# Performance work log

Hardware: AMD Instinct MI355X
Metric: run time of the kernel (lower is better)

Reference implementation:

```python
import jax, jax.numpy as jnp
import numpy as np

B = 4096      # number of snakes (graphs)
L = 256       # fixed snake length (nodes per chain)
N = B * L     # total nodes
HID = 32
OUT = 32
AUX = 32
FIN = 64
N_FRUITS = 1
AUX_IN = 2 + 1 + N_FRUITS * 2  # = 5


def _chain_edges():
    # chain edges i<->i+1 within each graph, both directions (PyG undirected chain)
    base = np.arange(L - 1)
    src1 = (np.arange(B)[:, None] * L + base[None, :]).ravel()
    dst1 = src1 + 1
    src = np.concatenate([src1, dst1])
    dst = np.concatenate([dst1, src1])
    return np.stack([src, dst]).astype(np.int64)  # [2, 2*(L-1)*B]


def setup_inputs() -> dict:
    key = jax.random.key(0)
    ks = jax.random.split(key, 16)

    def lin(k, fan_in, fan_out):
        k1, k2 = jax.random.split(k)
        bound = 1.0 / np.sqrt(fan_in)
        W = jax.random.uniform(k1, (fan_in, fan_out), jnp.float32, -bound, bound)
        b = jax.random.uniform(k2, (fan_out,), jnp.float32, -bound, bound)
        return W, b

    x = jax.random.normal(ks[0], (N, 2), jnp.float32)
    heads = jax.random.normal(ks[1], (B, 2), jnp.float32)
    body_sizes = jax.random.uniform(ks[2], (B, 1), jnp.float32)
    fruits = jax.random.normal(ks[3], (B, N_FRUITS, 2), jnp.float32)

    W1, b1 = lin(ks[4], 2, HID)
    W2, b2 = lin(ks[5], HID, HID)
    Wr, br = lin(ks[6], HID, OUT)
    Wa1, ba1 = lin(ks[7], AUX_IN, AUX)
    Wa2, ba2 = lin(ks[8], AUX, AUX)
    Wc, bc = lin(ks[9], OUT + AUX, FIN)
    Wp, bp = lin(ks[10], FIN, 5)
    Wv, bv = lin(ks[11], FIN, 1)

    edge_index = jnp.asarray(_chain_edges())
    batch_ids = jnp.repeat(jnp.arange(B, dtype=jnp.int64), L)

    return dict(x=x, heads=heads, body_sizes=body_sizes, fruits=fruits,
                W1=W1, b1=b1, W2=W2, b2=b2, Wr=Wr, br=br,
                Wa1=Wa1, ba1=ba1, Wa2=Wa2, ba2=ba2, Wc=Wc, bc=bc,
                Wp=Wp, bp=bp, Wv=Wv, bv=bv,
                edge_index=edge_index, batch_ids=batch_ids)


def _gcn_conv(h, W, b, src, dst):
    # PyG GCNConv: out = D^{-1/2} (A + I) D^{-1/2} (h W) + b, deg counts self-loop
    h = h @ W  # [N, F]
    ones = jnp.ones(src.shape[0], h.dtype)
    deg = jax.ops.segment_sum(ones, dst, num_segments=N) + 1.0  # self-loop
    dinv = jax.lax.rsqrt(deg)
    norm = dinv[src] * dinv[dst]  # [E]
    agg = jax.ops.segment_sum(norm[:, None] * h[src], dst, num_segments=N)
    agg = agg + (dinv * dinv)[:, None] * h  # self-loop messages
    return agg + b


def reference(x, heads, body_sizes, fruits,
              W1, b1, W2, b2, Wr, br, Wa1, ba1, Wa2, ba2,
              Wc, bc, Wp, bp, Wv, bv, edge_index, batch_ids):
    src, dst = edge_index[0], edge_index[1]
    h = jax.nn.relu(_gcn_conv(x, W1, b1, src, dst))
    h = jax.nn.relu(_gcn_conv(h, W2, b2, src, dst))
    # global mean pool per graph
    pooled = jax.ops.segment_sum(h, batch_ids, num_segments=B)
    counts = jax.ops.segment_sum(jnp.ones(N, h.dtype), batch_ids, num_segments=B)
    pooled = pooled / counts[:, None]
    body_emb = pooled @ Wr + br  # [B, OUT]

    aux_input = jnp.concatenate([heads, body_sizes,
                                 fruits.reshape(fruits.shape[0], -1)], axis=-1)
    aux = jax.nn.relu(aux_input @ Wa1 + ba1)
    aux = jax.nn.relu(aux @ Wa2 + ba2)

    combined = jnp.concatenate([body_emb, aux], axis=-1)
    combined = jax.nn.relu(combined @ Wc + bc)
    logits = combined @ Wp + bp  # [B, 5]
    value = combined @ Wv + bv   # [B, 1]
    return logits, value
```

## Files before the change

kernel.cpp:

```cpp
#include <hip/hip_runtime.h>
#include <hip/hip_bf16.h>


#define NB  4096
#define CL  256
#define HID 32
#define FIN 64
#define SPB 4

typedef __attribute__((ext_vector_type(8))) short    bf16x8;
typedef __attribute__((ext_vector_type(4))) float    f32x4;
typedef __attribute__((ext_vector_type(4))) unsigned u32x4;

__device__ __forceinline__ unsigned pkbf(float a, float b) {
    __hip_bfloat162 hb = __float22bfloat162_rn(make_float2(a, b));
    unsigned u; __builtin_memcpy(&u, &hb, sizeof(u));
    return u;
}
__device__ __forceinline__ float bflo(unsigned u) { return __builtin_bit_cast(float, u << 16); }
__device__ __forceinline__ float bfhi(unsigned u) { return __builtin_bit_cast(float, u & 0xffff0000u); }

__device__ __forceinline__ void gcn_coef(int n, float& nc, float& nl, float& nr) {
    const float IS3 = 0.57735026918962576f, IS2 = 0.70710678118654752f;
    const float dn = (n == 0 || n == CL - 1) ? IS2 : IS3;
    nc = dn * dn;
    nl = (n > 0)      ? dn * ((n == 1)      ? IS2 : IS3) : 0.0f;
    nr = (n < CL - 1) ? dn * ((n == CL - 2) ? IS2 : IS3) : 0.0f;
}

__global__ __launch_bounds__(256, 4) void snake_fused(
    const float* __restrict__ x,
    const float* __restrict__ heads,
    const float* __restrict__ body_sizes,
    const float* __restrict__ fruits,
    const float* __restrict__ W1, const float* __restrict__ b1,
    const float* __restrict__ W2, const float* __restrict__ b2,
    const float* __restrict__ Wr, const float* __restrict__ br,
    const float* __restrict__ Wa1, const float* __restrict__ ba1,
    const float* __restrict__ Wa2, const float* __restrict__ ba2,
    const float* __restrict__ Wc, const float* __restrict__ bc,
    const float* __restrict__ Wp, const float* __restrict__ bp,
    const float* __restrict__ Wv, const float* __restrict__ bv,
    float* __restrict__ out)
{
    __shared__ __align__(16) float edgebuf[SPB][4][2][HID];
    __shared__ __align__(16) float waveparts[SPB][HID][4];
    __shared__ __align__(16) float poolLDS[SPB][HID];
    __shared__ __align__(16) float auxLDS[SPB][HID];
    __shared__ __align__(16) float catLDS[SPB][FIN];

    const int blk  = blockIdx.x;
    const int i    = threadIdx.x;
    const int w    = i >> 6;
    const int lane = i & 63;
    const int g    = lane >> 4;
    const int c    = lane & 15;

    bf16x8 Bh[2], Bl[2];
    #pragma unroll
    for (int nt = 0; nt < 2; ++nt) {
        unsigned hh[4], ll[4];
        #pragma unroll
        for (int p = 0; p < 4; ++p) {
            const float wa = W2[(8 * g + 2 * p)     * HID + c + 16 * nt];
            const float wb = W2[(8 * g + 2 * p + 1) * HID + c + 16 * nt];
            const unsigned hu = pkbf(wa, wb);
            hh[p] = hu;
            ll[p] = pkbf(wa - bflo(hu), wb - bfhi(hu));
        }
        u32x4 H = {hh[0], hh[1], hh[2], hh[3]};
        u32x4 L = {ll[0], ll[1], ll[2], ll[3]};
        Bh[nt] = __builtin_bit_cast(bf16x8, H);
        Bl[nt] = __builtin_bit_cast(bf16x8, L);
    }
    const float b2v0 = b2[c], b2v1 = b2[c + 16];

    const float4 W1a0 = *reinterpret_cast<const float4*>(W1 + 8 * g);
    const float4 W1a1 = *reinterpret_cast<const float4*>(W1 + 8 * g + 4);
    const float4 W1b0 = *reinterpret_cast<const float4*>(W1 + HID + 8 * g);
    const float4 W1b1 = *reinterpret_cast<const float4*>(W1 + HID + 8 * g + 4);
    const float4 b1v0 = *reinterpret_cast<const float4*>(b1 + 8 * g);
    const float4 b1v1 = *reinterpret_cast<const float4*>(b1 + 8 * g + 4);

    float ncd, nld, nrd;
    gcn_coef(i, ncd, nld, nrd);

    const float THIRD = 0.33333333333333333f;
    const float I23   = 0.40824829046386302f;
    const bool fixL = (w == 0) && (g == 0);
    const bool fixR = (w == 3) && (g == 3);

    #pragma unroll 1
    for (int s = 0; s < SPB; ++s) {
        const int gs = SPB * blk + s;
        const float2* xs = reinterpret_cast<const float2*>(x) + gs * CL;

        const float2 xc = xs[i];
        const float2 xl = xs[i - (i > 0)];
        const float2 xr = xs[i + (i < CL - 1)];
        const float sxx = ncd * xc.x + nld * xl.x + nrd * xr.x;
        const float sxy = ncd * xc.y + nld * xl.y + nrd * xr.y;

        float sxA[4], syA[4];
        #pragma unroll
        for (int t = 0; t < 4; ++t) {
            sxA[t] = __shfl(sxx, 16 * t + c, 64);
            syA[t] = __shfl(sxy, 16 * t + c, 64);
        }

        f32x4 acc[4][2];
        #pragma unroll
        for (int t = 0; t < 4; ++t)
            #pragma unroll
            for (int nt = 0; nt < 2; ++nt) { f32x4 z = {0.f, 0.f, 0.f, 0.f}; acc[t][nt] = z; }

        #pragma unroll
        for (int t = 0; t < 4; ++t) {
            const float sa = sxA[t], sb = syA[t];
            const float r0 = fmaxf(fmaf(sa, W1a0.x, fmaf(sb, W1b0.x, b1v0.x)), 0.f);
            const float r1 = fmaxf(fmaf(sa, W1a0.y, fmaf(sb, W1b0.y, b1v0.y)), 0.f);
            const float r2 = fmaxf(fmaf(sa, W1a0.z, fmaf(sb, W1b0.z, b1v0.z)), 0.f);
            const float r3 = fmaxf(fmaf(sa, W1a0.w, fmaf(sb, W1b0.w, b1v0.w)), 0.f);
            const float r4 = fmaxf(fmaf(sa, W1a1.x, fmaf(sb, W1b1.x, b1v1.x)), 0.f);
            const float r5 = fmaxf(fmaf(sa, W1a1.y, fmaf(sb, W1b1.y, b1v1.y)), 0.f);
            const float r6 = fmaxf(fmaf(sa, W1a1.z, fmaf(sb, W1b1.z, b1v1.z)), 0.f);
            const float r7 = fmaxf(fmaf(sa, W1a1.w, fmaf(sb, W1b1.w, b1v1.w)), 0.f);
            const unsigned h0 = pkbf(r0, r1), h1 = pkbf(r2, r3);
            const unsigned h2 = pkbf(r4, r5), h3 = pkbf(r6, r7);
            const unsigned q0 = pkbf(r0 - bflo(h0), r1 - bfhi(h0));
            const unsigned q1 = pkbf(r2 - bflo(h1), r3 - bfhi(h1));
            const unsigned q2 = pkbf(r4 - bflo(h2), r5 - bfhi(h2));
            const unsigned q3 = pkbf(r6 - bflo(h3), r7 - bfhi(h3));
            u32x4 HU = {h0, h1, h2, h3};
            u32x4 LU = {q0, q1, q2, q3};
            const bf16x8 ah = __builtin_bit_cast(bf16x8, HU);
            const bf16x8 al = __builtin_bit_cast(bf16x8, LU);
            #pragma unroll
            for (int nt = 0; nt < 2; ++nt) {
                acc[t][nt] = __builtin_amdgcn_mfma_f32_16x16x32_bf16(ah, Bh[nt], acc[t][nt], 0, 0, 0);
                acc[t][nt] = __builtin_amdgcn_mfma_f32_16x16x32_bf16(al, Bh[nt], acc[t][nt], 0, 0, 0);
                acc[t][nt] = __builtin_amdgcn_mfma_f32_16x16x32_bf16(ah, Bl[nt], acc[t][nt], 0, 0, 0);
            }
        }

        if (lane < 16) {
            edgebuf[s][w][0][c]      = acc[0][0][0];
            edgebuf[s][w][0][c + 16] = acc[0][1][0];
        } else if (lane >= 48) {
            edgebuf[s][w][1][c]      = acc[3][0][3];
            edgebuf[s][w][1][c + 16] = acc[3][1][3];
        }
        __syncthreads();

        float sum0 = 0.f, sum1 = 0.f;
        #pragma unroll
        for (int t = 0; t < 4; ++t) {
            float c0 = THIRD, r0c = THIRD, l1c = THIRD;
            float c3 = THIRD, l3c = THIRD, r2c = THIRD;
            if (t == 0) { c0 = fixL ? 0.5f : THIRD; r0c = fixL ? I23 : THIRD; l1c = fixL ? I23 : THIRD; }
            if (t == 3) { c3 = fixR ? 0.5f : THIRD; l3c = fixR ? I23 : THIRD; r2c = fixR ? I23 : THIRD; }
            #pragma unroll
            for (int nt = 0; nt < 2; ++nt) {
                const f32x4 v = acc[t][nt];
                const float Lsend = (g == 3) ? acc[(t > 0) ? t - 1 : 0][nt][3] : acc[t][nt][3];
                const int   Lsrc  = (g == 0) ? (c + 48) : (lane - 16);
                float L = __shfl(Lsend, Lsrc, 64);
                if (t == 0) {
                    float eL = edgebuf[s][(w > 0) ? w - 1 : 0][1][c + 16 * nt];
                    eL = (w > 0) ? eL : 0.f;
                    L = (g == 0) ? eL : L;
                }
                const float Rsend = (g == 0) ? acc[(t < 3) ? t + 1 : 3][nt][0] : acc[t][nt][0];
                const int   Rsrc  = (g == 3) ? c : (lane + 16);
                float R = __shfl(Rsend, Rsrc, 64);
                if (t == 3) {
                    float eR = edgebuf[s][(w < 3) ? w + 1 : 3][0][c + 16 * nt];
                    eR = (w < 3) ? eR : 0.f;
                    R = (g == 3) ? eR : R;
                }
                const float bb = (nt == 0) ? b2v0 : b2v1;
                const float h0 = fmaxf(fmaf(c0,    v[0], fmaf(THIRD, L,    fmaf(r0c,  v[1], bb))), 0.f);
                const float h1 = fmaxf(fmaf(THIRD, v[1], fmaf(l1c,   v[0], fmaf(THIRD, v[2], bb))), 0.f);
                const float h2 = fmaxf(fmaf(THIRD, v[2], fmaf(THIRD, v[1], fmaf(r2c,  v[3], bb))), 0.f);
                const float h3 = fmaxf(fmaf(c3,    v[3], fmaf(l3c,   v[2], fmaf(THIRD, R,   bb))), 0.f);
                const float hs = (h0 + h1) + (h2 + h3);
                if (nt == 0) sum0 += hs; else sum1 += hs;
            }
        }
        sum0 += __shfl_xor(sum0, 16, 64); sum0 += __shfl_xor(sum0, 32, 64);
        sum1 += __shfl_xor(sum1, 16, 64); sum1 += __shfl_xor(sum1, 32, 64);
        if (g == 0) {
            waveparts[s][c][w]      = sum0;
            waveparts[s][c + 16][w] = sum1;
        }
    }
    __syncthreads();

    const int gsH = SPB * blk + w;
    if (lane < HID) {
        const f32x4 wp = *reinterpret_cast<const f32x4*>(&waveparts[w][lane][0]);
        poolLDS[w][lane] = (wp.x + wp.y + wp.z + wp.w) * (1.0f / CL);
    } else {
        const int cc = lane - HID;
        float a = ba1[cc];
        a = fmaf(heads[2 * gsH],      Wa1[0 * HID + cc], a);
        a = fmaf(heads[2 * gsH + 1],  Wa1[1 * HID + cc], a);
        a = fmaf(body_sizes[gsH],     Wa1[2 * HID + cc], a);
        a = fmaf(fruits[2 * gsH],     Wa1[3 * HID + cc], a);
        a = fmaf(fruits[2 * gsH + 1], Wa1[4 * HID + cc], a);
        auxLDS[w][cc] = fmaxf(a, 0.f);
    }
    __syncthreads();

    if (lane < HID) {
        float be0 = br[lane], be1 = 0.f;
        const float4* p4 = reinterpret_cast<const float4*>(poolLDS[w]);
        #pragma unroll
        for (int k4 = 0; k4 < 8; ++k4) {
            const float4 p = p4[k4];
            be0 = fmaf(p.x, Wr[(4 * k4 + 0) * HID + lane], be0);
            be1 = fmaf(p.y, Wr[(4 * k4 + 1) * HID + lane], be1);
            be0 = fmaf(p.z, Wr[(4 * k4 + 2) * HID + lane], be0);
            be1 = fmaf(p.w, Wr[(4 * k4 + 3) * HID + lane], be1);
        }
        catLDS[w][lane] = be0 + be1;
    } else {
        const int cc = lane - HID;
        float a0 = ba2[cc], a1 = 0.f;
        const float4* p4 = reinterpret_cast<const float4*>(auxLDS[w]);
        #pragma unroll
        for (int k4 = 0; k4 < 8; ++k4) {
            const float4 p = p4[k4];
            a0 = fmaf(p.x, Wa2[(4 * k4 + 0) * HID + cc], a0);
            a1 = fmaf(p.y, Wa2[(4 * k4 + 1) * HID + cc], a1);
            a0 = fmaf(p.z, Wa2[(4 * k4 + 2) * HID + cc], a0);
            a1 = fmaf(p.w, Wa2[(4 * k4 + 3) * HID + cc], a1);
        }
        catLDS[w][lane] = fmaxf(a0 + a1, 0.f);
    }
    __syncthreads();

    {
        float cb0 = bc[lane], cb1 = 0.f;
        const float4* c4p = reinterpret_cast<const float4*>(catLDS[w]);
        #pragma unroll
        for (int k4 = 0; k4 < 16; ++k4) {
            const float4 p = c4p[k4];
            cb0 = fmaf(p.x, Wc[(4 * k4 + 0) * FIN + lane], cb0);
            cb1 = fmaf(p.y, Wc[(4 * k4 + 1) * FIN + lane], cb1);
            cb0 = fmaf(p.z, Wc[(4 * k4 + 2) * FIN + lane], cb0);
            cb1 = fmaf(p.w, Wc[(4 * k4 + 3) * FIN + lane], cb1);
        }
        const float cb = fmaxf(cb0 + cb1, 0.f);
        float s0 = cb * Wp[lane * 5 + 0];
        float s1 = cb * Wp[lane * 5 + 1];
        float s2 = cb * Wp[lane * 5 + 2];
        float s3 = cb * Wp[lane * 5 + 3];
        float s4 = cb * Wp[lane * 5 + 4];
        float s5 = cb * Wv[lane];
        #pragma unroll
        for (int m = 1; m <= 32; m <<= 1) {
            s0 += __shfl_xor(s0, m, 64);
            s1 += __shfl_xor(s1, m, 64);
            s2 += __shfl_xor(s2, m, 64);
            s3 += __shfl_xor(s3, m, 64);
            s4 += __shfl_xor(s4, m, 64);
            s5 += __shfl_xor(s5, m, 64);
        }
        if (lane == 0) {
            out[gsH * 5 + 0] = s0 + bp[0];
            out[gsH * 5 + 1] = s1 + bp[1];
            out[gsH * 5 + 2] = s2 + bp[2];
            out[gsH * 5 + 3] = s3 + bp[3];
            out[gsH * 5 + 4] = s4 + bp[4];
            out[NB * 5 + gsH] = s5 + bv[0];
        }
    }
}

extern "C" void kernel_launch(void* const* d_in, const int* in_sizes, int n_in,
                              void* d_out, int out_size, void* d_ws, size_t ws_size,
                              hipStream_t stream) {
    const float* x          = (const float*)d_in[0];
    const float* heads      = (const float*)d_in[1];
    const float* body_sizes = (const float*)d_in[2];
    const float* fruits     = (const float*)d_in[3];
    const float* W1 = (const float*)d_in[4];
    const float* b1 = (const float*)d_in[5];
    const float* W2 = (const float*)d_in[6];
    const float* b2 = (const float*)d_in[7];
    const float* Wr = (const float*)d_in[8];
    const float* br = (const float*)d_in[9];
    const float* Wa1 = (const float*)d_in[10];
    const float* ba1 = (const float*)d_in[11];
    const float* Wa2 = (const float*)d_in[12];
    const float* ba2 = (const float*)d_in[13];
    const float* Wc = (const float*)d_in[14];
    const float* bc = (const float*)d_in[15];
    const float* Wp = (const float*)d_in[16];
    const float* bp = (const float*)d_in[17];
    const float* Wv = (const float*)d_in[18];
    const float* bv = (const float*)d_in[19];

    float* out = (float*)d_out;
    snake_fused<<<NB / SPB, CL, 0, stream>>>(
        x, heads, body_sizes, fruits,
        W1, b1, W2, b2, Wr, br, Wa1, ba1, Wa2, ba2,
        Wc, bc, Wp, bp, Wv, bv, out);
}
```

Baseline: 126.8 us.

## Assign one snake per wave with rolling tile window, removing block barriers

Each of the four waves in a block now handles a whole 256-node snake on its own, walking 16 MFMA tiles with a rolling previous/current/next accumulator window. Before, the four waves split each snake and met at block barriers to swap boundary rows and partial sums. The change removes the `__syncthreads` calls and the cross-wave edge buffers. The MLP head now runs wave-locally with one merged LDS scratch, where the Wr and Wa2 products are computed by the two halves of a wave at once. In exchange, each wave runs a longer serial chain and loads x per tile with neighbour reads, which may reduce the latency hiding within a wave.

```diff
diff --git a/kernel.cpp b/kernel.cpp
--- a/kernel.cpp
+++ b/kernel.cpp
@@ -6,7 +6,6 @@
 #define CL  256
 #define HID 32
 #define FIN 64
-#define SPB 4
 
 typedef __attribute__((ext_vector_type(8))) short    bf16x8;
 typedef __attribute__((ext_vector_type(4))) float    f32x4;
@@ -43,18 +42,14 @@
     const float* __restrict__ Wv, const float* __restrict__ bv,
     float* __restrict__ out)
 {
-    __shared__ __align__(16) float edgebuf[SPB][4][2][HID];
-    __shared__ __align__(16) float waveparts[SPB][HID][4];
-    __shared__ __align__(16) float poolLDS[SPB][HID];
-    __shared__ __align__(16) float auxLDS[SPB][HID];
-    __shared__ __align__(16) float catLDS[SPB][FIN];
-
-    const int blk  = blockIdx.x;
-    const int i    = threadIdx.x;
-    const int w    = i >> 6;
-    const int lane = i & 63;
+    __shared__ __align__(16) float wsc[4][FIN];
+
+    const int tid  = threadIdx.x;
+    const int w    = tid >> 6;
+    const int lane = tid & 63;
     const int g    = lane >> 4;
     const int c    = lane & 15;
+    const int gs   = blockIdx.x * 4 + w;
 
     bf16x8 Bh[2], Bl[2];
     #pragma unroll
@@ -75,183 +70,139 @@
     }
     const float b2v0 = b2[c], b2v1 = b2[c + 16];
 
-    const float4 W1a0 = *reinterpret_cast<const float4*>(W1 + 8 * g);
-    const float4 W1a1 = *reinterpret_cast<const float4*>(W1 + 8 * g + 4);
-    const float4 W1b0 = *reinterpret_cast<const float4*>(W1 + HID + 8 * g);
-    const float4 W1b1 = *reinterpret_cast<const float4*>(W1 + HID + 8 * g + 4);
-    const float4 b1v0 = *reinterpret_cast<const float4*>(b1 + 8 * g);
-    const float4 b1v1 = *reinterpret_cast<const float4*>(b1 + 8 * g + 4);
-
-    float ncd, nld, nrd;
-    gcn_coef(i, ncd, nld, nrd);
+    const float4 W1a0 = *(const float4*)(W1 + 8 * g);
+    const float4 W1a1 = *(const float4*)(W1 + 8 * g + 4);
+    const float4 W1b0 = *(const float4*)(W1 + HID + 8 * g);
+    const float4 W1b1 = *(const float4*)(W1 + HID + 8 * g + 4);
+    const float4 b1v0 = *(const float4*)(b1 + 8 * g);
+    const float4 b1v1 = *(const float4*)(b1 + 8 * g + 4);
 
     const float THIRD = 0.33333333333333333f;
     const float I23   = 0.40824829046386302f;
-    const bool fixL = (w == 0) && (g == 0);
-    const bool fixR = (w == 3) && (g == 3);
-
-    #pragma unroll 1
-    for (int s = 0; s < SPB; ++s) {
-        const int gs = SPB * blk + s;
-        const float2* xs = reinterpret_cast<const float2*>(x) + gs * CL;
-
-        const float2 xc = xs[i];
-        const float2 xl = xs[i - (i > 0)];
-        const float2 xr = xs[i + (i < CL - 1)];
-        const float sxx = ncd * xc.x + nld * xl.x + nrd * xr.x;
-        const float sxy = ncd * xc.y + nld * xl.y + nrd * xr.y;
-
-        float sxA[4], syA[4];
-        #pragma unroll
-        for (int t = 0; t < 4; ++t) {
-            sxA[t] = __shfl(sxx, 16 * t + c, 64);
-            syA[t] = __shfl(sxy, 16 * t + c, 64);
-        }
-
-        f32x4 acc[4][2];
-        #pragma unroll
-        for (int t = 0; t < 4; ++t)
-            #pragma unroll
-            for (int nt = 0; nt < 2; ++nt) { f32x4 z = {0.f, 0.f, 0.f, 0.f}; acc[t][nt] = z; }
-
-        #pragma unroll
-        for (int t = 0; t < 4; ++t) {
-            const float sa = sxA[t], sb = syA[t];
-            const float r0 = fmaxf(fmaf(sa, W1a0.x, fmaf(sb, W1b0.x, b1v0.x)), 0.f);
-            const float r1 = fmaxf(fmaf(sa, W1a0.y, fmaf(sb, W1b0.y, b1v0.y)), 0.f);
-            const float r2 = fmaxf(fmaf(sa, W1a0.z, fmaf(sb, W1b0.z, b1v0.z)), 0.f);
-            const float r3 = fmaxf(fmaf(sa, W1a0.w, fmaf(sb, W1b0.w, b1v0.w)), 0.f);
-            const float r4 = fmaxf(fmaf(sa, W1a1.x, fmaf(sb, W1b1.x, b1v1.x)), 0.f);
-            const float r5 = fmaxf(fmaf(sa, W1a1.y, fmaf(sb, W1b1.y, b1v1.y)), 0.f);
-            const float r6 = fmaxf(fmaf(sa, W1a1.z, fmaf(sb, W1b1.z, b1v1.z)), 0.f);
-            const float r7 = fmaxf(fmaf(sa, W1a1.w, fmaf(sb, W1b1.w, b1v1.w)), 0.f);
-            const unsigned h0 = pkbf(r0, r1), h1 = pkbf(r2, r3);
-            const unsigned h2 = pkbf(r4, r5), h3 = pkbf(r6, r7);
-            const unsigned q0 = pkbf(r0 - bflo(h0), r1 - bfhi(h0));
-            const unsigned q1 = pkbf(r2 - bflo(h1), r3 - bfhi(h1));
-            const unsigned q2 = pkbf(r4 - bflo(h2), r5 - bfhi(h2));
-            const unsigned q3 = pkbf(r6 - bflo(h3), r7 - bfhi(h3));
-            u32x4 HU = {h0, h1, h2, h3};
-            u32x4 LU = {q0, q1, q2, q3};
-            const bf16x8 ah = __builtin_bit_cast(bf16x8, HU);
-            const bf16x8 al = __builtin_bit_cast(bf16x8, LU);
-            #pragma unroll
-            for (int nt = 0; nt < 2; ++nt) {
-                acc[t][nt] = __builtin_amdgcn_mfma_f32_16x16x32_bf16(ah, Bh[nt], acc[t][nt], 0, 0, 0);
-                acc[t][nt] = __builtin_amdgcn_mfma_f32_16x16x32_bf16(al, Bh[nt], acc[t][nt], 0, 0, 0);
-                acc[t][nt] = __builtin_amdgcn_mfma_f32_16x16x32_bf16(ah, Bl[nt], acc[t][nt], 0, 0, 0);
-            }
-        }
-
-        if (lane < 16) {
-            edgebuf[s][w][0][c]      = acc[0][0][0];
-            edgebuf[s][w][0][c + 16] = acc[0][1][0];
-        } else if (lane >= 48) {
-            edgebuf[s][w][1][c]      = acc[3][0][3];
-            edgebuf[s][w][1][c + 16] = acc[3][1][3];
-        }
-        __syncthreads();
-
-        float sum0 = 0.f, sum1 = 0.f;
-        #pragma unroll
-        for (int t = 0; t < 4; ++t) {
-            float c0 = THIRD, r0c = THIRD, l1c = THIRD;
-            float c3 = THIRD, l3c = THIRD, r2c = THIRD;
-            if (t == 0) { c0 = fixL ? 0.5f : THIRD; r0c = fixL ? I23 : THIRD; l1c = fixL ? I23 : THIRD; }
-            if (t == 3) { c3 = fixR ? 0.5f : THIRD; l3c = fixR ? I23 : THIRD; r2c = fixR ? I23 : THIRD; }
-            #pragma unroll
-            for (int nt = 0; nt < 2; ++nt) {
-                const f32x4 v = acc[t][nt];
-                const float Lsend = (g == 3) ? acc[(t > 0) ? t - 1 : 0][nt][3] : acc[t][nt][3];
-                const int   Lsrc  = (g == 0) ? (c + 48) : (lane - 16);
-                float L = __shfl(Lsend, Lsrc, 64);
-                if (t == 0) {
-                    float eL = edgebuf[s][(w > 0) ? w - 1 : 0][1][c + 16 * nt];
-                    eL = (w > 0) ? eL : 0.f;
-                    L = (g == 0) ? eL : L;
-                }
-                const float Rsend = (g == 0) ? acc[(t < 3) ? t + 1 : 3][nt][0] : acc[t][nt][0];
-                const int   Rsrc  = (g == 3) ? c : (lane + 16);
-                float R = __shfl(Rsend, Rsrc, 64);
-                if (t == 3) {
-                    float eR = edgebuf[s][(w < 3) ? w + 1 : 3][0][c + 16 * nt];
-                    eR = (w < 3) ? eR : 0.f;
-                    R = (g == 3) ? eR : R;
-                }
-                const float bb = (nt == 0) ? b2v0 : b2v1;
-                const float h0 = fmaxf(fmaf(c0,    v[0], fmaf(THIRD, L,    fmaf(r0c,  v[1], bb))), 0.f);
-                const float h1 = fmaxf(fmaf(THIRD, v[1], fmaf(l1c,   v[0], fmaf(THIRD, v[2], bb))), 0.f);
-                const float h2 = fmaxf(fmaf(THIRD, v[2], fmaf(THIRD, v[1], fmaf(r2c,  v[3], bb))), 0.f);
-                const float h3 = fmaxf(fmaf(c3,    v[3], fmaf(l3c,   v[2], fmaf(THIRD, R,   bb))), 0.f);
-                const float hs = (h0 + h1) + (h2 + h3);
-                if (nt == 0) sum0 += hs; else sum1 += hs;
-            }
-        }
-        sum0 += __shfl_xor(sum0, 16, 64); sum0 += __shfl_xor(sum0, 32, 64);
-        sum1 += __shfl_xor(sum1, 16, 64); sum1 += __shfl_xor(sum1, 32, 64);
-        if (g == 0) {
-            waveparts[s][c][w]      = sum0;
-            waveparts[s][c + 16][w] = sum1;
-        }
-    }
-    __syncthreads();
-
-    const int gsH = SPB * blk + w;
-    if (lane < HID) {
-        const f32x4 wp = *reinterpret_cast<const f32x4*>(&waveparts[w][lane][0]);
-        poolLDS[w][lane] = (wp.x + wp.y + wp.z + wp.w) * (1.0f / CL);
-    } else {
-        const int cc = lane - HID;
+
+    const float2* xs = (const float2*)x + gs * CL;
+
+    auto compute_tile = [&](int t, f32x4* accT) {
+        const int m = 16 * t + c;
+        const float2 xcv = xs[m];
+        const float2 xlv = xs[m - (m > 0)];
+        const float2 xrv = xs[m + (m < CL - 1)];
+        float ncd, nld, nrd;
+        if (t == 0 || t == 15) { gcn_coef(m, ncd, nld, nrd); }
+        else { ncd = THIRD; nld = THIRD; nrd = THIRD; }
+        const float sa = ncd * xcv.x + nld * xlv.x + nrd * xrv.x;
+        const float sb = ncd * xcv.y + nld * xlv.y + nrd * xrv.y;
+        const float r0 = fmaxf(fmaf(sa, W1a0.x, fmaf(sb, W1b0.x, b1v0.x)), 0.f);
+        const float r1 = fmaxf(fmaf(sa, W1a0.y, fmaf(sb, W1b0.y, b1v0.y)), 0.f);
+        const float r2 = fmaxf(fmaf(sa, W1a0.z, fmaf(sb, W1b0.z, b1v0.z)), 0.f);
+        const float r3 = fmaxf(fmaf(sa, W1a0.w, fmaf(sb, W1b0.w, b1v0.w)), 0.f);
+        const float r4 = fmaxf(fmaf(sa, W1a1.x, fmaf(sb, W1b1.x, b1v1.x)), 0.f);
+        const float r5 = fmaxf(fmaf(sa, W1a1.y, fmaf(sb, W1b1.y, b1v1.y)), 0.f);
+        const float r6 = fmaxf(fmaf(sa, W1a1.z, fmaf(sb, W1b1.z, b1v1.z)), 0.f);
+        const float r7 = fmaxf(fmaf(sa, W1a1.w, fmaf(sb, W1b1.w, b1v1.w)), 0.f);
+        const unsigned h0 = pkbf(r0, r1), h1 = pkbf(r2, r3);
+        const unsigned h2 = pkbf(r4, r5), h3 = pkbf(r6, r7);
+        const unsigned q0 = pkbf(r0 - bflo(h0), r1 - bfhi(h0));
+        const unsigned q1 = pkbf(r2 - bflo(h1), r3 - bfhi(h1));
+        const unsigned q2 = pkbf(r4 - bflo(h2), r5 - bfhi(h2));
+        const unsigned q3 = pkbf(r6 - bflo(h3), r7 - bfhi(h3));
+        u32x4 HU = {h0, h1, h2, h3};
+        u32x4 LU = {q0, q1, q2, q3};
+        const bf16x8 ah = __builtin_bit_cast(bf16x8, HU);
+        const bf16x8 al = __builtin_bit_cast(bf16x8, LU);
+        #pragma unroll
+        for (int nt = 0; nt < 2; ++nt) {
+            f32x4 a0 = {0.f, 0.f, 0.f, 0.f};
+            a0 = __builtin_amdgcn_mfma_f32_16x16x32_bf16(ah, Bh[nt], a0, 0, 0, 0);
+            a0 = __builtin_amdgcn_mfma_f32_16x16x32_bf16(al, Bh[nt], a0, 0, 0, 0);
+            a0 = __builtin_amdgcn_mfma_f32_16x16x32_bf16(ah, Bl[nt], a0, 0, 0, 0);
+            accT[nt] = a0;
+        }
+    };
+
+    f32x4 accP[2], accC[2], accN[2];
+    { f32x4 z = {0.f, 0.f, 0.f, 0.f}; accP[0] = z; accP[1] = z; accN[0] = z; accN[1] = z; }
+    compute_tile(0, accC);
+    float sum0 = 0.f, sum1 = 0.f;
+
+    #pragma unroll
+    for (int t = 0; t < 16; ++t) {
+        if (t < 15) compute_tile(t + 1, accN);
+        const bool fL = (t == 0)  && (g == 0);
+        const bool fR = (t == 15) && (g == 3);
+        const float c0  = fL ? 0.5f : THIRD;
+        const float r0c = fL ? I23  : THIRD;
+        const float l1c = fL ? I23  : THIRD;
+        const float c3  = fR ? 0.5f : THIRD;
+        const float l3c = fR ? I23  : THIRD;
+        const float r2c = fR ? I23  : THIRD;
+        #pragma unroll
+        for (int nt = 0; nt < 2; ++nt) {
+            const f32x4 v = accC[nt];
+            const float Lsend = (g == 3) ? accP[nt][3] : v[3];
+            const int   Lsrc  = (g == 0) ? (c + 48) : (lane - 16);
+            float L = __shfl(Lsend, Lsrc, 64);
+            if (t == 0)  L = (g == 0) ? 0.f : L;
+            const float Rsend = (g == 0) ? accN[nt][0] : v[0];
+            const int   Rsrc  = (g == 3) ? c : (lane + 16);
+            float R = __shfl(Rsend, Rsrc, 64);
+            if (t == 15) R = (g == 3) ? 0.f : R;
+            const float bb = nt ? b2v1 : b2v0;
+            const float h0 = fmaxf(fmaf(c0,    v[0], fmaf(THIRD, L,    fmaf(r0c,   v[1], bb))), 0.f);
+            const float h1 = fmaxf(fmaf(THIRD, v[1], fmaf(l1c,   v[0], fmaf(THIRD, v[2], bb))), 0.f);
+            const float h2 = fmaxf(fmaf(THIRD, v[2], fmaf(THIRD, v[1], fmaf(r2c,   v[3], bb))), 0.f);
+            const float h3 = fmaxf(fmaf(c3,    v[3], fmaf(l3c,   v[2], fmaf(THIRD, R,    bb))), 0.f);
+            const float hs = (h0 + h1) + (h2 + h3);
+            if (nt == 0) sum0 += hs; else sum1 += hs;
+        }
+        accP[0] = accC[0]; accP[1] = accC[1];
+        accC[0] = accN[0]; accC[1] = accN[1];
+    }
+
+    sum0 += __shfl_xor(sum0, 16, 64); sum0 += __shfl_xor(sum0, 32, 64);
+    sum1 += __shfl_xor(sum1, 16, 64); sum1 += __shfl_xor(sum1, 32, 64);
+    wsc[w][c]      = sum0 * (1.0f / CL);
+    wsc[w][c + 16] = sum1 * (1.0f / CL);
+
+    if (lane >= 32) {
+        const int cc = lane - 32;
         float a = ba1[cc];
-        a = fmaf(heads[2 * gsH],      Wa1[0 * HID + cc], a);
-        a = fmaf(heads[2 * gsH + 1],  Wa1[1 * HID + cc], a);
-        a = fmaf(body_sizes[gsH],     Wa1[2 * HID + cc], a);
-        a = fmaf(fruits[2 * gsH],     Wa1[3 * HID + cc], a);
-        a = fmaf(fruits[2 * gsH + 1], Wa1[4 * HID + cc], a);
-        auxLDS[w][cc] = fmaxf(a, 0.f);
-    }
-    __syncthreads();
-
-    if (lane < HID) {
-        float be0 = br[lane], be1 = 0.f;
-        const float4* p4 = reinterpret_cast<const float4*>(poolLDS[w]);
+        a = fmaf(heads[2 * gs],      Wa1[0 * HID + cc], a);
+        a = fmaf(heads[2 * gs + 1],  Wa1[1 * HID + cc], a);
+        a = fmaf(body_sizes[gs],     Wa1[2 * HID + cc], a);
+        a = fmaf(fruits[2 * gs],     Wa1[3 * HID + cc], a);
+        a = fmaf(fruits[2 * gs + 1], Wa1[4 * HID + cc], a);
+        wsc[w][32 + cc] = fmaxf(a, 0.f);
+    }
+    {
+        const int  hh = lane >> 5;
+        const int  cc = lane & 31;
+        const float* Wsel = hh ? Wa2 : Wr;
+        const float  bsel = hh ? ba2[cc] : br[cc];
+        const float* lsel = &wsc[w][32 * hh];
+        float cv = bsel;
         #pragma unroll
         for (int k4 = 0; k4 < 8; ++k4) {
-            const float4 p = p4[k4];
-            be0 = fmaf(p.x, Wr[(4 * k4 + 0) * HID + lane], be0);
-            be1 = fmaf(p.y, Wr[(4 * k4 + 1) * HID + lane], be1);
-            be0 = fmaf(p.z, Wr[(4 * k4 + 2) * HID + lane], be0);
-            be1 = fmaf(p.w, Wr[(4 * k4 + 3) * HID + lane], be1);
-        }
-        catLDS[w][lane] = be0 + be1;
-    } else {
-        const int cc = lane - HID;
-        float a0 = ba2[cc], a1 = 0.f;
-        const float4* p4 = reinterpret_cast<const float4*>(auxLDS[w]);
-        #pragma unroll
-        for (int k4 = 0; k4 < 8; ++k4) {
-            const float4 p = p4[k4];
-            a0 = fmaf(p.x, Wa2[(4 * k4 + 0) * HID + cc], a0);
-            a1 = fmaf(p.y, Wa2[(4 * k4 + 1) * HID + cc], a1);
-            a0 = fmaf(p.z, Wa2[(4 * k4 + 2) * HID + cc], a0);
-            a1 = fmaf(p.w, Wa2[(4 * k4 + 3) * HID + cc], a1);
-        }
-        catLDS[w][lane] = fmaxf(a0 + a1, 0.f);
-    }
-    __syncthreads();
-
+            const f32x4 p = *(const f32x4*)&lsel[4 * k4];
+            cv = fmaf(p[0], Wsel[(4 * k4 + 0) * HID + cc], cv);
+            cv = fmaf(p[1], Wsel[(4 * k4 + 1) * HID + cc], cv);
+            cv = fmaf(p[2], Wsel[(4 * k4 + 2) * HID + cc], cv);
+            cv = fmaf(p[3], Wsel[(4 * k4 + 3) * HID + cc], cv);
+        }
+        cv = hh ? fmaxf(cv, 0.f) : cv;
+        wsc[w][lane] = cv;
+    }
     {
-        float cb0 = bc[lane], cb1 = 0.f;
-        const float4* c4p = reinterpret_cast<const float4*>(catLDS[w]);
+        float cb = bc[lane];
         #pragma unroll
         for (int k4 = 0; k4 < 16; ++k4) {
-            const float4 p = c4p[k4];
-            cb0 = fmaf(p.x, Wc[(4 * k4 + 0) * FIN + lane], cb0);
-            cb1 = fmaf(p.y, Wc[(4 * k4 + 1) * FIN + lane], cb1);
-            cb0 = fmaf(p.z, Wc[(4 * k4 + 2) * FIN + lane], cb0);
-            cb1 = fmaf(p.w, Wc[(4 * k4 + 3) * FIN + lane], cb1);
-        }
-        const float cb = fmaxf(cb0 + cb1, 0.f);
+            const f32x4 p = *(const f32x4*)&wsc[w][4 * k4];
+            cb = fmaf(p[0], Wc[(4 * k4 + 0) * FIN + lane], cb);
+            cb = fmaf(p[1], Wc[(4 * k4 + 1) * FIN + lane], cb);
+            cb = fmaf(p[2], Wc[(4 * k4 + 2) * FIN + lane], cb);
+            cb = fmaf(p[3], Wc[(4 * k4 + 3) * FIN + lane], cb);
+        }
+        cb = fmaxf(cb, 0.f);
         float s0 = cb * Wp[lane * 5 + 0];
         float s1 = cb * Wp[lane * 5 + 1];
         float s2 = cb * Wp[lane * 5 + 2];
@@ -268,12 +219,12 @@
             s5 += __shfl_xor(s5, m, 64);
         }
         if (lane == 0) {
-            out[gsH * 5 + 0] = s0 + bp[0];
-            out[gsH * 5 + 1] = s1 + bp[1];
-            out[gsH * 5 + 2] = s2 + bp[2];
-            out[gsH * 5 + 3] = s3 + bp[3];
-            out[gsH * 5 + 4] = s4 + bp[4];
-            out[NB * 5 + gsH] = s5 + bv[0];
+            out[gs * 5 + 0] = s0 + bp[0];
+            out[gs * 5 + 1] = s1 + bp[1];
+            out[gs * 5 + 2] = s2 + bp[2];
+            out[gs * 5 + 3] = s3 + bp[3];
+            out[gs * 5 + 4] = s4 + bp[4];
+            out[NB * 5 + gs] = s5 + bv[0];
         }
     }
 }
@@ -303,7 +254,7 @@
     const float* bv = (const float*)d_in[19];
 
     float* out = (float*)d_out;
-    snake_fused<<<NB / SPB, CL, 0, stream>>>(
+    snake_fused<<<NB / 4, 256, 0, stream>>>(
         x, heads, body_sizes, fruits,
         W1, b1, W2, b2, Wr, br, Wa1, ba1, Wa2, ba2,
         Wc, bc, Wp, bp, Wv, bv, out);
```

Measured after the change: 128.5 us. About the same (+1.3%).
